# Performance work log

Hardware: AMD Instinct MI355X
Metric: run time of the kernel (lower is better)

## Reference

```python
import jax, jax.numpy as jnp
import numpy as np

B, C, HEADS, D, DKQ = 1024, 512, 8, 64, 8
DV = C // HEADS                 # 64, dim_head_v
QKVC = DV + 2 * DKQ             # 80, qkv channels per head
EPS = 1e-5


def _bn(x, g, b, m, v):
    # eval-mode batchnorm, channel axis = 1
    shp = (1, -1) + (1,) * (x.ndim - 2)
    scale = g.reshape(shp) / jnp.sqrt(v.reshape(shp) + EPS)
    return (x - m.reshape(shp)) * scale + b.reshape(shp)


def _rel_index():
    i = np.arange(D)
    # key_index - query_index + D - 1, row-major flatten -> (D*D,)
    return jnp.asarray((i[:, None] - i[None, :] + D - 1).reshape(-1))


def setup_inputs() -> dict:
    key = jax.random.key(0)
    ks = jax.random.split(key, 16)
    O = HEADS * QKVC
    d = {
        "x": jax.random.normal(ks[0], (B, C, D), jnp.float32),
        "conv_w": jax.random.normal(ks[1], (O, C), jnp.float32) * 0.02,
        "bn1_g": jax.random.normal(ks[2], (O,), jnp.float32) * 0.1 + 1.0,
        "bn1_b": jax.random.normal(ks[3], (O,), jnp.float32) * 0.1,
        "bn1_m": jax.random.normal(ks[4], (O,), jnp.float32) * 0.1,
        "bn1_v": jax.random.uniform(ks[5], (O,), jnp.float32) * 0.5 + 0.5,
        "rel": jax.random.normal(ks[6], (QKVC, 2 * D - 1), jnp.float32),
        "bn2_g": jax.random.normal(ks[7], (3 * HEADS,), jnp.float32) * 0.1 + 1.0,
        "bn2_b": jax.random.normal(ks[8], (3 * HEADS,), jnp.float32) * 0.1,
        "bn2_m": jax.random.normal(ks[9], (3 * HEADS,), jnp.float32) * 0.1,
        "bn2_v": jax.random.uniform(ks[10], (3 * HEADS,), jnp.float32) * 0.5 + 0.5,
        "bn3_g": jax.random.normal(ks[11], (2 * C,), jnp.float32) * 0.1 + 1.0,
        "bn3_b": jax.random.normal(ks[12], (2 * C,), jnp.float32) * 0.1,
        "bn3_m": jax.random.normal(ks[13], (2 * C,), jnp.float32) * 0.1,
        "bn3_v": jax.random.uniform(ks[14], (2 * C,), jnp.float32) * 0.5 + 0.5,
    }
    return d


def reference(x, conv_w, bn1_g, bn1_b, bn1_m, bn1_v, rel,
              bn2_g, bn2_b, bn2_m, bn2_v, bn3_g, bn3_b, bn3_m, bn3_v):
    # 1x1 conv1d + BN1d: [B, O, D]
    qkv = jnp.einsum('oc,bcd->bod', conv_w, x)
    qkv = _bn(qkv, bn1_g, bn1_b, bn1_m, bn1_v)
    # rearrange 'b (q h) d -> b h q d' with q=QKVC, h=HEADS (channel = q*H + h)
    qkv = qkv.reshape(B, QKVC, HEADS, D).transpose(0, 2, 1, 3)  # [B,H,QKVC,D]
    q = qkv[:, :, :DKQ]                # [B,H,DKQ,D]
    k = qkv[:, :, DKQ:2 * DKQ]         # [B,H,DKQ,D]
    v = qkv[:, :, 2 * DKQ:]            # [B,H,DV,D]

    # relative positional embeddings gathered from table
    emb = rel[:, _rel_index()].reshape(QKVC, D, D)
    r_q, r_k, r_v = emb[:DKQ], emb[DKQ:2 * DKQ], emb[2 * DKQ:]

    qr = jnp.einsum('bhid,idj->bhdj', q, r_q)
    kr = jnp.einsum('bhid,idj->bhdj', k, r_k)
    dots = jnp.einsum('bhid,bhij->bhdj', q, k)

    # rearrange 'n b h d j -> b (h n) d j'  (channel = h*3 + n)
    stacked = jnp.stack([qr, kr, dots], axis=2).reshape(B, 3 * HEADS, D, D)
    stacked = _bn(stacked, bn2_g, bn2_b, bn2_m, bn2_v)
    norm_dots = stacked.reshape(B, HEADS, 3, D, D).sum(axis=2)  # [B,H,D,D]

    attn = jax.nn.softmax(norm_dots, axis=-1)
    out = jnp.einsum('bhdj,bhij->bhid', attn, v)      # [B,H,DV,D]
    kv = jnp.einsum('bhdj,idj->bhid', attn, r_v)      # [B,H,DV,D]

    # rearrange 'n b h i d -> b (n h i) d'  (channel = n*H*DV + h*DV + i)
    st = jnp.stack([kv, out], axis=1).reshape(B, 2 * HEADS * DV, D)
    st = _bn(st, bn3_g, bn3_b, bn3_m, bn3_v)
    return st.reshape(B, 2, HEADS * DV, D).sum(axis=1)  # [B,C,D]
```

## Files before the change

kernel.cpp:

```cpp
#include <hip/hip_runtime.h>
#include <hip/hip_bf16.h>

#define B_    1024
#define C_    512
#define H_    8
#define D_    64
#define EPS_  1e-5f

typedef __attribute__((ext_vector_type(4))) float f32x4;
typedef __attribute__((ext_vector_type(8))) short bf16x8;
typedef __attribute__((ext_vector_type(8))) unsigned short u16x8;

__device__ __forceinline__ float bf2f(unsigned short h) {
    union { unsigned int u; float f; } c;
    c.u = ((unsigned int)h) << 16;
    return c.f;
}
__device__ __forceinline__ unsigned short f2bf(float f) {
    __hip_bfloat16 h = __float2bfloat16(f);
    return *reinterpret_cast<unsigned short*>(&h);
}

__global__ __launch_bounds__(256) void k0_wconv(
    const float* __restrict__ w, unsigned short* __restrict__ wf)
{
    int t = blockIdx.x * 256 + threadIdx.x;
    int o  = t >> 6;
    int c0 = (t & 63) * 8;
    const float* src = w + (size_t)o * C_ + c0;
    u16x8 p;
#pragma unroll
    for (int e = 0; e < 8; ++e) p[e] = f2bf(src[e]);
    int f = (o >> 4) * 16 + (c0 >> 5);
    int l = (o & 15) | (((c0 >> 3) & 3) << 4);
    *reinterpret_cast<u16x8*>(&wf[(size_t)f * 512 + l * 8]) = p;
}

__global__ __launch_bounds__(256) void k0_tables(
    const float* __restrict__ rel,
    const float* __restrict__ g2, const float* __restrict__ v2,
    const float* __restrict__ g3, const float* __restrict__ v3,
    unsigned short* __restrict__ relB, unsigned short* __restrict__ relvA)
{
    int tid = blockIdx.x * 256 + threadIdx.x;
    if (tid < 4096) {
        int h = tid >> 9, uf = (tid >> 6) & 7, l = tid & 63;
        int u = uf * 16 + (l & 15);
        int g = l >> 4;
        float sq = g2[3*h]     * rsqrtf(v2[3*h]     + EPS_);
        float sk = g2[3*h + 1] * rsqrtf(v2[3*h + 1] + EPS_);
        u16x8 p;
#pragma unroll
        for (int e = 0; e < 8; ++e) {
            int s = g * 8 + e;
            float val = 0.f;
            if (u < 127 && s < 16)
                val = (s < 8 ? sq : sk) * rel[s * 127 + u];
            p[e] = f2bf(val);
        }
        *reinterpret_cast<u16x8*>(&relB[(size_t)tid * 8]) = p;
    } else if (tid < 4096 + 8192) {
        int t2 = tid - 4096;
        int h = t2 >> 10, iF = (t2 >> 8) & 3, tt = (t2 >> 6) & 3, l = t2 & 63;
        int i = iF * 16 + (l & 15);
        int c3 = h * 64 + i;
        float scl = g3[c3] * rsqrtf(v3[c3] + EPS_);
        const float* rrow = rel + (size_t)(16 + i) * 127;
        u16x8 p;
#pragma unroll
        for (int e = 0; e < 8; ++e) {
            int u = (l >> 4) * 8 + e + 32 * tt;
            p[e] = f2bf((u < 127) ? scl * rrow[u] : 0.f);
        }
        *reinterpret_cast<u16x8*>(&relvA[(size_t)t2 * 8]) = p;
    }
}

#define LDW1 40

__global__ __launch_bounds__(512) void k1_gemm(
    const float* __restrict__ x, const unsigned short* __restrict__ wf,
    const float* __restrict__ g1, const float* __restrict__ b1,
    const float* __restrict__ m1, const float* __restrict__ v1,
    const float* __restrict__ g3, const float* __restrict__ v3,
    unsigned short* __restrict__ qkA, unsigned short* __restrict__ vB)
{
    __shared__ unsigned short xt[32 * LDW1];
    __shared__ float ssc[640], ssh[640];

    const int tid = threadIdx.x;
    const int b   = blockIdx.x >> 1;
    const int dh  = blockIdx.x & 1;
    const int d0  = dh * 32;

    for (int t = tid; t < 640; t += 512) {
        float sc = g1[t] * rsqrtf(v1[t] + EPS_);
        float sh = b1[t] - m1[t] * sc;
        int cc = t >> 3, hh = t & 7;
        if (cc >= 16) {
            int c3 = 512 + hh * 64 + (cc - 16);
            float f = g3[c3] * rsqrtf(v3[c3] + EPS_);
            sc *= f; sh *= f;
        }
        ssc[t] = sc;
        ssh[t] = sh;
    }

    const int lane = tid & 63;
    const int wv   = tid >> 6;
    const int wrow = wv * 80;
    const int lm   = lane & 15;
    const int lk   = (lane >> 4) * 8;

    f32x4 acc[5][2];
#pragma unroll
    for (int i = 0; i < 5; ++i)
#pragma unroll
        for (int j = 0; j < 2; ++j) acc[i][j] = (f32x4){0.f, 0.f, 0.f, 0.f};

    const float* xb = x + (size_t)b * C_ * D_;
    const int skp = tid >> 5;
    const int sdd = tid & 31;

    for (int kk = 0; kk < C_; kk += 32) {
        __syncthreads();
        bf16x8 af[5];
#pragma unroll
        for (int fm = 0; fm < 5; ++fm) {
            size_t f = (size_t)((wv * 5 + fm) * 16 + (kk >> 5)) * 512;
            af[fm] = *reinterpret_cast<const bf16x8*>(&wf[f + lane * 8]);
        }
        {
            float a0 = xb[(kk + 2 * skp) * 64 + d0 + sdd];
            float a1 = xb[(kk + 2 * skp + 1) * 64 + d0 + sdd];
            unsigned int pk = (unsigned int)f2bf(a0) | ((unsigned int)f2bf(a1) << 16);
            *reinterpret_cast<unsigned int*>(&xt[sdd * LDW1 + 2 * skp]) = pk;
        }
        __syncthreads();

        bf16x8 bfr[2];
#pragma unroll
        for (int fn = 0; fn < 2; ++fn)
            bfr[fn] = *reinterpret_cast<const bf16x8*>(&xt[(fn * 16 + lm) * LDW1 + lk]);
#pragma unroll
        for (int fm = 0; fm < 5; ++fm)
#pragma unroll
            for (int fn = 0; fn < 2; ++fn)
                acc[fm][fn] = __builtin_amdgcn_mfma_f32_16x16x32_bf16(
                    af[fm], bfr[fn], acc[fm][fn], 0, 0, 0);
    }

    const int r0 = (lane >> 4) * 4;
#pragma unroll
    for (int fm = 0; fm < 5; ++fm) {
#pragma unroll
        for (int fn = 0; fn < 2; ++fn) {
            int d = d0 + fn * 16 + lm;
#pragma unroll
            for (int r = 0; r < 4; ++r) {
                int o = wrow + fm * 16 + r0 + r;
                int cc = o >> 3, hh = o & 7;
                float val = acc[fm][fn][r] * ssc[o] + ssh[o];
                unsigned short bv = f2bf(val);
                if (cc < 8)
                    qkA[(((size_t)b * 8 + hh) * 4 + (d >> 4)) * 512 + (d & 15) * 8 + cc] = bv;
                else if (cc < 16)
                    qkA[(((size_t)b * 8 + hh) * 4 + (d >> 4)) * 512 + ((d & 15) + 16) * 8 + (cc - 8)] = bv;
                else
                    vB[((size_t)(b * 8 + hh) * 64 + (cc - 16)) * 64 + d] = bv;
            }
        }
    }
    for (int z = tid; z < 2048; z += 512) {
        int hm  = z >> 7;
        int off = z & 127;
        int hh  = hm >> 1;
        int mf  = dh * 2 + (hm & 1);
        unsigned int* p = reinterpret_cast<unsigned int*>(
            qkA + (((size_t)b * 8 + hh) * 4 + mf) * 512 + 256);
        p[off] = 0u;
    }
}

#define SGP 84
#define SA  72
#define RLD 136

__global__ __launch_bounds__(256) void k2_attn(
    const unsigned short* __restrict__ qkA, const unsigned short* __restrict__ vB,
    const unsigned short* __restrict__ relB, const unsigned short* __restrict__ relvA,
    const float* __restrict__ g2, const float* __restrict__ v2,
    const float* __restrict__ g3, const float* __restrict__ b3,
    const float* __restrict__ m3, const float* __restrict__ v3,
    float* __restrict__ outp)
{
    __shared__ float          SGb[64 * SGP];
    __shared__ unsigned short attn[64 * SA];
    __shared__ unsigned short A2[64 * RLD];
    __shared__ float sh3[64];

    const int tid  = threadIdx.x;
    const int b    = blockIdx.x >> 3;
    const int h    = blockIdx.x & 7;
    const int lane = tid & 63;
    const int w    = tid >> 6;
    const int lmm  = lane & 15;
    const int lg   = lane >> 4;

    const unsigned short* qbase = qkA + ((size_t)(b * 8 + h) * 4) * 512;

    for (int i = tid; i < 64 * RLD / 2; i += 256)
        reinterpret_cast<unsigned int*>(A2)[i] = 0u;
    if (tid < 64) {
        int c = h * 64 + tid;
        float sa = g3[c] * rsqrtf(v3[c] + EPS_);
        float sb = g3[512 + c] * rsqrtf(v3[512 + c] + EPS_);
        sh3[tid] = (b3[c] - m3[c] * sa) + (b3[512 + c] - m3[512 + c] * sb);
    }
    const float s_dt = g2[3 * h + 2] * rsqrtf(v2[3 * h + 2] + EPS_);

    bf16x8 aA = *reinterpret_cast<const bf16x8*>(&qbase[w * 512 + lane * 8]);
    bf16x8 zv = {0, 0, 0, 0, 0, 0, 0, 0};
    bf16x8 kBf[4];
#pragma unroll
    for (int jf = 0; jf < 4; ++jf) {
        kBf[jf] = zv;
        if (lane < 16)
            kBf[jf] = *reinterpret_cast<const bf16x8*>(&qbase[jf * 512 + (lane + 16) * 8]);
    }
    bf16x8 rBf[8];
#pragma unroll
    for (int uf = 0; uf < 8; ++uf)
        rBf[uf] = *reinterpret_cast<const bf16x8*>(&relB[(size_t)(h * 8 + uf) * 512 + lane * 8]);

    f32x4 dotsAcc[4];
#pragma unroll
    for (int jf = 0; jf < 4; ++jf)
        dotsAcc[jf] = __builtin_amdgcn_mfma_f32_16x16x32_bf16(
            aA, kBf[jf], (f32x4){0.f, 0.f, 0.f, 0.f}, 0, 0, 0);
    f32x4 sgAcc[8];
#pragma unroll
    for (int uf = 0; uf < 8; ++uf)
        sgAcc[uf] = __builtin_amdgcn_mfma_f32_16x16x32_bf16(
            aA, rBf[uf], (f32x4){0.f, 0.f, 0.f, 0.f}, 0, 0, 0);

#pragma unroll
    for (int uf = 0; uf < 8; ++uf) {
#pragma unroll
        for (int r = 0; r < 4; ++r) {
            int d = (w << 4) + (lg << 2) + r;
            int t = uf * 16 + lmm - d + 15;
            if (t >= 0 && t < 79)
                SGb[d * SGP + t] = sgAcc[uf][r];
        }
    }
    __syncthreads();

#pragma unroll
    for (int r = 0; r < 4; ++r) {
        int d = (w << 4) + (lg << 2) + r;
        const float* sgr = &SGb[d * SGP];
        float sc0 = s_dt * dotsAcc[0][r] + sgr[78 - lmm];
        float sc1 = s_dt * dotsAcc[1][r] + sgr[62 - lmm];
        float sc2 = s_dt * dotsAcc[2][r] + sgr[46 - lmm];
        float sc3 = s_dt * dotsAcc[3][r] + sgr[30 - lmm];
        float mx = fmaxf(fmaxf(sc0, sc1), fmaxf(sc2, sc3));
        mx = fmaxf(mx, __shfl_xor(mx, 1));
        mx = fmaxf(mx, __shfl_xor(mx, 2));
        mx = fmaxf(mx, __shfl_xor(mx, 4));
        mx = fmaxf(mx, __shfl_xor(mx, 8));
        float e0 = __expf(sc0 - mx), e1 = __expf(sc1 - mx);
        float e2 = __expf(sc2 - mx), e3 = __expf(sc3 - mx);
        float sum = (e0 + e1) + (e2 + e3);
        sum += __shfl_xor(sum, 1);
        sum += __shfl_xor(sum, 2);
        sum += __shfl_xor(sum, 4);
        sum += __shfl_xor(sum, 8);
        float inv = 1.f / sum;
        unsigned short p0 = f2bf(e0 * inv), p1 = f2bf(e1 * inv);
        unsigned short p2 = f2bf(e2 * inv), p3 = f2bf(e3 * inv);
        attn[d * SA + lmm]      = p0;
        attn[d * SA + 16 + lmm] = p1;
        attn[d * SA + 32 + lmm] = p2;
        attn[d * SA + 48 + lmm] = p3;
        A2[d * RLD + 63 + d - lmm] = p0;
        A2[d * RLD + 47 + d - lmm] = p1;
        A2[d * RLD + 31 + d - lmm] = p2;
        A2[d * RLD + 15 + d - lmm] = p3;
    }

    const int lk8  = lg * 8;
    const int irow = (w << 4) + lmm;
    const unsigned short* vbase = vB + (size_t)(b * 8 + h) * 4096;
    bf16x8 av0 = *reinterpret_cast<const bf16x8*>(&vbase[irow * 64 + lk8]);
    bf16x8 av1 = *reinterpret_cast<const bf16x8*>(&vbase[irow * 64 + 32 + lk8]);
    bf16x8 rvA[4];
#pragma unroll
    for (int t = 0; t < 4; ++t)
        rvA[t] = *reinterpret_cast<const bf16x8*>(
            &relvA[(size_t)(((h * 4 + w) * 4 + t)) * 512 + lane * 8]);

    __syncthreads();

    f32x4 acc[4];
#pragma unroll
    for (int nf = 0; nf < 4; ++nf) acc[nf] = (f32x4){0.f, 0.f, 0.f, 0.f};

#pragma unroll
    for (int nf = 0; nf < 4; ++nf) {
        const unsigned short* arow = &attn[(nf * 16 + lmm) * SA + lk8];
        acc[nf] = __builtin_amdgcn_mfma_f32_16x16x32_bf16(
            av0, *reinterpret_cast<const bf16x8*>(&arow[0]), acc[nf], 0, 0, 0);
        acc[nf] = __builtin_amdgcn_mfma_f32_16x16x32_bf16(
            av1, *reinterpret_cast<const bf16x8*>(&arow[32]), acc[nf], 0, 0, 0);
        const unsigned short* a2row = &A2[(nf * 16 + lmm) * RLD + lk8];
        acc[nf] = __builtin_amdgcn_mfma_f32_16x16x32_bf16(
            rvA[0], *reinterpret_cast<const bf16x8*>(&a2row[0]), acc[nf], 0, 0, 0);
        acc[nf] = __builtin_amdgcn_mfma_f32_16x16x32_bf16(
            rvA[1], *reinterpret_cast<const bf16x8*>(&a2row[32]), acc[nf], 0, 0, 0);
        acc[nf] = __builtin_amdgcn_mfma_f32_16x16x32_bf16(
            rvA[2], *reinterpret_cast<const bf16x8*>(&a2row[64]), acc[nf], 0, 0, 0);
        acc[nf] = __builtin_amdgcn_mfma_f32_16x16x32_bf16(
            rvA[3], *reinterpret_cast<const bf16x8*>(&a2row[96]), acc[nf], 0, 0, 0);
    }

    float* op = outp + ((size_t)b * 512 + h * 64) * 64;
    const int r0 = lg * 4;
#pragma unroll
    for (int r = 0; r < 4; ++r) {
        int i = (w << 4) + r0 + r;
        float sh = sh3[i];
#pragma unroll
        for (int nf = 0; nf < 4; ++nf)
            op[(size_t)i * 64 + nf * 16 + lmm] = acc[nf][r] + sh;
    }
}

extern "C" void kernel_launch(void* const* d_in, const int* in_sizes, int n_in,
                              void* d_out, int out_size, void* d_ws, size_t ws_size,
                              hipStream_t stream) {
    (void)in_sizes; (void)n_in; (void)out_size; (void)ws_size;
    const float* x   = (const float*)d_in[0];
    const float* w   = (const float*)d_in[1];
    const float* g1  = (const float*)d_in[2];
    const float* b1  = (const float*)d_in[3];
    const float* m1  = (const float*)d_in[4];
    const float* v1  = (const float*)d_in[5];
    const float* rel = (const float*)d_in[6];
    const float* g2  = (const float*)d_in[7];
    const float* b2  = (const float*)d_in[8];  (void)b2;
    const float* m2  = (const float*)d_in[9];  (void)m2;
    const float* v2  = (const float*)d_in[10];
    const float* g3  = (const float*)d_in[11];
    const float* b3  = (const float*)d_in[12];
    const float* m3  = (const float*)d_in[13];
    const float* v3  = (const float*)d_in[14];
    float* out = (float*)d_out;

    unsigned short* wfrag = (unsigned short*)d_ws;
    unsigned short* relB  = (unsigned short*)((char*)d_ws + 655360);
    unsigned short* relvA = (unsigned short*)((char*)d_ws + 720896);
    unsigned short* qkA   = (unsigned short*)((char*)d_ws + 1048576);
    unsigned short* vB    = (unsigned short*)((char*)d_ws + 1048576 + (size_t)33554432);

    hipLaunchKernelGGL(k0_wconv, dim3(160), dim3(256), 0, stream, w, wfrag);
    hipLaunchKernelGGL(k0_tables, dim3(48), dim3(256), 0, stream,
                       rel, g2, v2, g3, v3, relB, relvA);
    hipLaunchKernelGGL(k1_gemm, dim3(2048), dim3(512), 0, stream,
                       x, wfrag, g1, b1, m1, v1, g3, v3, qkA, vB);
    hipLaunchKernelGGL(k2_attn, dim3(8192), dim3(256), 0, stream,
                       qkA, vB, relB, relvA, g2, v2, g3, b3, m3, v3, out);
}
```

Measured before the change: 203.4 us.

## Widen k1 GEMM tile to full D per block with double-buffered LDS prefetch

The projection GEMM now has each block cover all 64 positions of a batch instead of half. The weight fragments loaded per k-step are therefore reused across twice as many MFMAs, and the grid is halved. The K loop moves to 64-wide steps with a double-buffered LDS tile. The next x tile is prefetched into registers with vectorized float4 loads while the current one is computed, which cuts barriers per K. In exchange, accumulator registers double, which may lower occupancy, and there are fewer blocks to spread across the CUs.

```diff
diff --git a/kernel.cpp b/kernel.cpp
--- a/kernel.cpp
+++ b/kernel.cpp
@@ -76,7 +76,7 @@
     }
 }
 
-#define LDW1 40
+#define LDW1 72
 
 __global__ __launch_bounds__(512) void k1_gemm(
     const float* __restrict__ x, const unsigned short* __restrict__ wf,
@@ -85,13 +85,11 @@
     const float* __restrict__ g3, const float* __restrict__ v3,
     unsigned short* __restrict__ qkA, unsigned short* __restrict__ vB)
 {
-    __shared__ unsigned short xt[32 * LDW1];
+    __shared__ unsigned short xt[2][64 * LDW1];
     __shared__ float ssc[640], ssh[640];
 
     const int tid = threadIdx.x;
-    const int b   = blockIdx.x >> 1;
-    const int dh  = blockIdx.x & 1;
-    const int d0  = dh * 32;
+    const int b   = blockIdx.x;
 
     for (int t = tid; t < 640; t += 512) {
         float sc = g1[t] * rsqrtf(v1[t] + EPS_);
@@ -108,57 +106,76 @@
 
     const int lane = tid & 63;
     const int wv   = tid >> 6;
-    const int wrow = wv * 80;
     const int lm   = lane & 15;
-    const int lk   = (lane >> 4) * 8;
-
-    f32x4 acc[5][2];
+    const int lg   = lane >> 4;
+
+    const float* xb = x + (size_t)b * C_ * D_;
+    const int cp = tid >> 4;
+    const int c4 = (tid & 15) * 4;
+
+    f32x4 acc[5][4];
 #pragma unroll
     for (int i = 0; i < 5; ++i)
 #pragma unroll
-        for (int j = 0; j < 2; ++j) acc[i][j] = (f32x4){0.f, 0.f, 0.f, 0.f};
-
-    const float* xb = x + (size_t)b * C_ * D_;
-    const int skp = tid >> 5;
-    const int sdd = tid & 31;
-
-    for (int kk = 0; kk < C_; kk += 32) {
+        for (int j = 0; j < 4; ++j) acc[i][j] = (f32x4){0.f, 0.f, 0.f, 0.f};
+
+    {
+        f32x4 a = *reinterpret_cast<const f32x4*>(&xb[(2 * cp) * 64 + c4]);
+        f32x4 c = *reinterpret_cast<const f32x4*>(&xb[(2 * cp + 1) * 64 + c4]);
+#pragma unroll
+        for (int j = 0; j < 4; ++j) {
+            unsigned int pk = (unsigned int)f2bf(a[j]) | ((unsigned int)f2bf(c[j]) << 16);
+            *reinterpret_cast<unsigned int*>(&xt[0][(c4 + j) * LDW1 + 2 * cp]) = pk;
+        }
+    }
+    __syncthreads();
+
+    int cur = 0;
+    for (int kt = 0; kt < 8; ++kt) {
+        f32x4 pa, pc;
+        if (kt < 7) {
+            pa = *reinterpret_cast<const f32x4*>(&xb[((kt + 1) * 64 + 2 * cp) * 64 + c4]);
+            pc = *reinterpret_cast<const f32x4*>(&xb[((kt + 1) * 64 + 2 * cp + 1) * 64 + c4]);
+        }
+#pragma unroll
+        for (int ks = 0; ks < 2; ++ks) {
+            bf16x8 af[5];
+#pragma unroll
+            for (int fm = 0; fm < 5; ++fm) {
+                size_t f = (size_t)((wv * 5 + fm) * 16 + kt * 2 + ks) * 512;
+                af[fm] = *reinterpret_cast<const bf16x8*>(&wf[f + lane * 8]);
+            }
+            bf16x8 bfr[4];
+#pragma unroll
+            for (int fn = 0; fn < 4; ++fn)
+                bfr[fn] = *reinterpret_cast<const bf16x8*>(
+                    &xt[cur][(fn * 16 + lm) * LDW1 + ks * 32 + lg * 8]);
+#pragma unroll
+            for (int fm = 0; fm < 5; ++fm)
+#pragma unroll
+                for (int fn = 0; fn < 4; ++fn)
+                    acc[fm][fn] = __builtin_amdgcn_mfma_f32_16x16x32_bf16(
+                        af[fm], bfr[fn], acc[fm][fn], 0, 0, 0);
+        }
+        if (kt < 7) {
+#pragma unroll
+            for (int j = 0; j < 4; ++j) {
+                unsigned int pk = (unsigned int)f2bf(pa[j]) | ((unsigned int)f2bf(pc[j]) << 16);
+                *reinterpret_cast<unsigned int*>(&xt[cur ^ 1][(c4 + j) * LDW1 + 2 * cp]) = pk;
+            }
+        }
         __syncthreads();
-        bf16x8 af[5];
-#pragma unroll
-        for (int fm = 0; fm < 5; ++fm) {
-            size_t f = (size_t)((wv * 5 + fm) * 16 + (kk >> 5)) * 512;
-            af[fm] = *reinterpret_cast<const bf16x8*>(&wf[f + lane * 8]);
-        }
-        {
-            float a0 = xb[(kk + 2 * skp) * 64 + d0 + sdd];
-            float a1 = xb[(kk + 2 * skp + 1) * 64 + d0 + sdd];
-            unsigned int pk = (unsigned int)f2bf(a0) | ((unsigned int)f2bf(a1) << 16);
-            *reinterpret_cast<unsigned int*>(&xt[sdd * LDW1 + 2 * skp]) = pk;
-        }
-        __syncthreads();
-
-        bf16x8 bfr[2];
-#pragma unroll
-        for (int fn = 0; fn < 2; ++fn)
-            bfr[fn] = *reinterpret_cast<const bf16x8*>(&xt[(fn * 16 + lm) * LDW1 + lk]);
-#pragma unroll
-        for (int fm = 0; fm < 5; ++fm)
-#pragma unroll
-            for (int fn = 0; fn < 2; ++fn)
-                acc[fm][fn] = __builtin_amdgcn_mfma_f32_16x16x32_bf16(
-                    af[fm], bfr[fn], acc[fm][fn], 0, 0, 0);
-    }
-
-    const int r0 = (lane >> 4) * 4;
+        cur ^= 1;
+    }
+
 #pragma unroll
     for (int fm = 0; fm < 5; ++fm) {
 #pragma unroll
-        for (int fn = 0; fn < 2; ++fn) {
-            int d = d0 + fn * 16 + lm;
+        for (int fn = 0; fn < 4; ++fn) {
+            int d = fn * 16 + lm;
 #pragma unroll
             for (int r = 0; r < 4; ++r) {
-                int o = wrow + fm * 16 + r0 + r;
+                int o = wv * 80 + fm * 16 + lg * 4 + r;
                 int cc = o >> 3, hh = o & 7;
                 float val = acc[fm][fn][r] * ssc[o] + ssh[o];
                 unsigned short bv = f2bf(val);
@@ -171,11 +188,10 @@
             }
         }
     }
-    for (int z = tid; z < 2048; z += 512) {
-        int hm  = z >> 7;
+    for (int z = tid; z < 4096; z += 512) {
+        int hh  = z >> 9;
+        int mf  = (z >> 7) & 3;
         int off = z & 127;
-        int hh  = hm >> 1;
-        int mf  = dh * 2 + (hm & 1);
         unsigned int* p = reinterpret_cast<unsigned int*>(
             qkA + (((size_t)b * 8 + hh) * 4 + mf) * 512 + 256);
         p[off] = 0u;
@@ -366,7 +382,7 @@
     hipLaunchKernelGGL(k0_wconv, dim3(160), dim3(256), 0, stream, w, wfrag);
     hipLaunchKernelGGL(k0_tables, dim3(48), dim3(256), 0, stream,
                        rel, g2, v2, g3, v3, relB, relvA);
-    hipLaunchKernelGGL(k1_gemm, dim3(2048), dim3(512), 0, stream,
+    hipLaunchKernelGGL(k1_gemm, dim3(1024), dim3(512), 0, stream,
                        x, wfrag, g1, b1, m1, v1, g3, v3, qkA, vB);
     hipLaunchKernelGGL(k2_attn, dim3(8192), dim3(256), 0, stream,
                        qkA, vB, relB, relvA, g2, v2, g3, b3, m3, v3, out);
```

New measurement: 192.1 us. 5.5% less time.

## Double-buffer k1 GEMM tiles, split rows across blocks, compact qkA layout

Applied to the files above, without the earlier changes.

The conv GEMM kernel now uses 256-thread blocks that each cover half of the 640 output rows, so twice as many blocks are launched. The K loop is fully unrolled with register double-buffering of weight fragments and an LDS double buffer for x, prefetching the next tile while MFMAs run. It also uses a single barrier per step with an explicit lgkmcnt wait. The qkA layout drops the zero-padded upper half of each fragment, halving that buffer and removing the zero-fill pass; the attention kernel instead zero-fills the missing lanes in registers. In exchange, the x tile is read from global twice as often, and the hand-written barrier must keep LDS ordering correct.

```diff
diff --git a/kernel.cpp b/kernel.cpp
--- a/kernel.cpp
+++ b/kernel.cpp
@@ -7,6 +7,7 @@
 #define D_    64
 #define EPS_  1e-5f
 
+typedef __attribute__((ext_vector_type(2))) float f32x2;
 typedef __attribute__((ext_vector_type(4))) float f32x4;
 typedef __attribute__((ext_vector_type(8))) short bf16x8;
 typedef __attribute__((ext_vector_type(8))) unsigned short u16x8;
@@ -20,6 +21,11 @@
     __hip_bfloat16 h = __float2bfloat16(f);
     return *reinterpret_cast<unsigned short*>(&h);
 }
+
+#define KBAR() do { \
+    asm volatile("s_waitcnt lgkmcnt(0)" ::: "memory"); \
+    __builtin_amdgcn_s_barrier(); \
+} while (0)
 
 __global__ __launch_bounds__(256) void k0_wconv(
     const float* __restrict__ w, unsigned short* __restrict__ wf)
@@ -78,25 +84,73 @@
 
 #define LDW1 40
 
-__global__ __launch_bounds__(512) void k1_gemm(
+struct K1Ctx {
+    const float* xb;
+    const unsigned short* wfw;
+    unsigned short (*xt)[32 * LDW1];
+    int lm, lg, cp, d2l, dcol0;
+};
+
+template<int KT>
+__device__ __forceinline__ void k1_step(const K1Ctx& c, f32x4 (&acc)[5][2],
+                                        bf16x8 (&afu)[5], bf16x8 (&afp)[5])
+{
+    if (KT < 15) {
+#pragma unroll
+        for (int fm = 0; fm < 5; ++fm)
+            afp[fm] = *reinterpret_cast<const bf16x8*>(
+                &c.wfw[(size_t)(fm * 16 + KT + 1) * 512]);
+    }
+    f32x2 pa, pb;
+    if (KT < 15) {
+        pa = *reinterpret_cast<const f32x2*>(
+            &c.xb[((KT + 1) * 32 + 2 * c.cp) * 64 + c.dcol0 + c.d2l]);
+        pb = *reinterpret_cast<const f32x2*>(
+            &c.xb[((KT + 1) * 32 + 2 * c.cp + 1) * 64 + c.dcol0 + c.d2l]);
+    }
+    bf16x8 bfr[2];
+#pragma unroll
+    for (int fn = 0; fn < 2; ++fn)
+        bfr[fn] = *reinterpret_cast<const bf16x8*>(
+            &c.xt[KT & 1][(fn * 16 + c.lm) * LDW1 + c.lg * 8]);
+#pragma unroll
+    for (int fm = 0; fm < 5; ++fm)
+#pragma unroll
+        for (int fn = 0; fn < 2; ++fn)
+            acc[fm][fn] = __builtin_amdgcn_mfma_f32_16x16x32_bf16(
+                afu[fm], bfr[fn], acc[fm][fn], 0, 0, 0);
+    if (KT < 15) {
+        unsigned int p0 = (unsigned int)f2bf(pa[0]) | ((unsigned int)f2bf(pb[0]) << 16);
+        unsigned int p1 = (unsigned int)f2bf(pa[1]) | ((unsigned int)f2bf(pb[1]) << 16);
+        *reinterpret_cast<unsigned int*>(
+            &c.xt[(KT & 1) ^ 1][c.d2l * LDW1 + 2 * c.cp]) = p0;
+        *reinterpret_cast<unsigned int*>(
+            &c.xt[(KT & 1) ^ 1][(c.d2l + 1) * LDW1 + 2 * c.cp]) = p1;
+    }
+    KBAR();
+}
+
+__global__ __launch_bounds__(256, 4) void k1_gemm(
     const float* __restrict__ x, const unsigned short* __restrict__ wf,
     const float* __restrict__ g1, const float* __restrict__ b1,
     const float* __restrict__ m1, const float* __restrict__ v1,
     const float* __restrict__ g3, const float* __restrict__ v3,
     unsigned short* __restrict__ qkA, unsigned short* __restrict__ vB)
 {
-    __shared__ unsigned short xt[32 * LDW1];
-    __shared__ float ssc[640], ssh[640];
-
-    const int tid = threadIdx.x;
-    const int b   = blockIdx.x >> 1;
-    const int dh  = blockIdx.x & 1;
-    const int d0  = dh * 32;
-
-    for (int t = tid; t < 640; t += 512) {
-        float sc = g1[t] * rsqrtf(v1[t] + EPS_);
-        float sh = b1[t] - m1[t] * sc;
-        int cc = t >> 3, hh = t & 7;
+    __shared__ unsigned short xt[2][32 * LDW1];
+    __shared__ float ssc[320], ssh[320];
+
+    const int tid  = threadIdx.x;
+    const int b    = blockIdx.x >> 2;
+    const int mh   = (blockIdx.x >> 1) & 1;
+    const int dh   = blockIdx.x & 1;
+    const int row0 = mh * 320;
+
+    for (int t = tid; t < 320; t += 256) {
+        int o = row0 + t;
+        float sc = g1[o] * rsqrtf(v1[o] + EPS_);
+        float sh = b1[o] - m1[o] * sc;
+        int cc = o >> 3, hh = o & 7;
         if (cc >= 16) {
             int c3 = 512 + hh * 64 + (cc - 16);
             float f = g3[c3] * rsqrtf(v3[c3] + EPS_);
@@ -108,9 +162,16 @@
 
     const int lane = tid & 63;
     const int wv   = tid >> 6;
-    const int wrow = wv * 80;
-    const int lm   = lane & 15;
-    const int lk   = (lane >> 4) * 8;
+
+    K1Ctx c;
+    c.xb    = x + (size_t)b * C_ * D_;
+    c.wfw   = wf + (size_t)(mh * 20 + wv * 5) * 16 * 512 + lane * 8;
+    c.xt    = xt;
+    c.lm    = lane & 15;
+    c.lg    = lane >> 4;
+    c.cp    = tid >> 4;
+    c.d2l   = (tid & 15) * 2;
+    c.dcol0 = dh * 32;
 
     f32x4 acc[5][2];
 #pragma unroll
@@ -118,67 +179,60 @@
 #pragma unroll
         for (int j = 0; j < 2; ++j) acc[i][j] = (f32x4){0.f, 0.f, 0.f, 0.f};
 
-    const float* xb = x + (size_t)b * C_ * D_;
-    const int skp = tid >> 5;
-    const int sdd = tid & 31;
-
-    for (int kk = 0; kk < C_; kk += 32) {
-        __syncthreads();
-        bf16x8 af[5];
-#pragma unroll
-        for (int fm = 0; fm < 5; ++fm) {
-            size_t f = (size_t)((wv * 5 + fm) * 16 + (kk >> 5)) * 512;
-            af[fm] = *reinterpret_cast<const bf16x8*>(&wf[f + lane * 8]);
-        }
-        {
-            float a0 = xb[(kk + 2 * skp) * 64 + d0 + sdd];
-            float a1 = xb[(kk + 2 * skp + 1) * 64 + d0 + sdd];
-            unsigned int pk = (unsigned int)f2bf(a0) | ((unsigned int)f2bf(a1) << 16);
-            *reinterpret_cast<unsigned int*>(&xt[sdd * LDW1 + 2 * skp]) = pk;
-        }
-        __syncthreads();
-
-        bf16x8 bfr[2];
-#pragma unroll
-        for (int fn = 0; fn < 2; ++fn)
-            bfr[fn] = *reinterpret_cast<const bf16x8*>(&xt[(fn * 16 + lm) * LDW1 + lk]);
-#pragma unroll
-        for (int fm = 0; fm < 5; ++fm)
-#pragma unroll
-            for (int fn = 0; fn < 2; ++fn)
-                acc[fm][fn] = __builtin_amdgcn_mfma_f32_16x16x32_bf16(
-                    af[fm], bfr[fn], acc[fm][fn], 0, 0, 0);
-    }
-
-    const int r0 = (lane >> 4) * 4;
+    bf16x8 afA[5], afB[5];
+#pragma unroll
+    for (int fm = 0; fm < 5; ++fm)
+        afA[fm] = *reinterpret_cast<const bf16x8*>(&c.wfw[(size_t)(fm * 16) * 512]);
+    {
+        f32x2 a = *reinterpret_cast<const f32x2*>(
+            &c.xb[(2 * c.cp) * 64 + c.dcol0 + c.d2l]);
+        f32x2 d = *reinterpret_cast<const f32x2*>(
+            &c.xb[(2 * c.cp + 1) * 64 + c.dcol0 + c.d2l]);
+        unsigned int p0 = (unsigned int)f2bf(a[0]) | ((unsigned int)f2bf(d[0]) << 16);
+        unsigned int p1 = (unsigned int)f2bf(a[1]) | ((unsigned int)f2bf(d[1]) << 16);
+        *reinterpret_cast<unsigned int*>(&xt[0][c.d2l * LDW1 + 2 * c.cp]) = p0;
+        *reinterpret_cast<unsigned int*>(&xt[0][(c.d2l + 1) * LDW1 + 2 * c.cp]) = p1;
+    }
+    KBAR();
+
+    k1_step< 0>(c, acc, afA, afB);
+    k1_step< 1>(c, acc, afB, afA);
+    k1_step< 2>(c, acc, afA, afB);
+    k1_step< 3>(c, acc, afB, afA);
+    k1_step< 4>(c, acc, afA, afB);
+    k1_step< 5>(c, acc, afB, afA);
+    k1_step< 6>(c, acc, afA, afB);
+    k1_step< 7>(c, acc, afB, afA);
+    k1_step< 8>(c, acc, afA, afB);
+    k1_step< 9>(c, acc, afB, afA);
+    k1_step<10>(c, acc, afA, afB);
+    k1_step<11>(c, acc, afB, afA);
+    k1_step<12>(c, acc, afA, afB);
+    k1_step<13>(c, acc, afB, afA);
+    k1_step<14>(c, acc, afA, afB);
+    k1_step<15>(c, acc, afB, afA);
+
+    const int lm = c.lm, lg = c.lg;
 #pragma unroll
     for (int fm = 0; fm < 5; ++fm) {
 #pragma unroll
         for (int fn = 0; fn < 2; ++fn) {
-            int d = d0 + fn * 16 + lm;
+            int d = dh * 32 + fn * 16 + lm;
 #pragma unroll
             for (int r = 0; r < 4; ++r) {
-                int o = wrow + fm * 16 + r0 + r;
+                int rl = wv * 80 + fm * 16 + lg * 4 + r;
+                int o  = row0 + rl;
                 int cc = o >> 3, hh = o & 7;
-                float val = acc[fm][fn][r] * ssc[o] + ssh[o];
+                float val = acc[fm][fn][r] * ssc[rl] + ssh[rl];
                 unsigned short bv = f2bf(val);
                 if (cc < 8)
-                    qkA[(((size_t)b * 8 + hh) * 4 + (d >> 4)) * 512 + (d & 15) * 8 + cc] = bv;
+                    qkA[(((size_t)b * 8 + hh) * 4 + (d >> 4)) * 256 + (d & 15) * 8 + cc] = bv;
                 else if (cc < 16)
-                    qkA[(((size_t)b * 8 + hh) * 4 + (d >> 4)) * 512 + ((d & 15) + 16) * 8 + (cc - 8)] = bv;
+                    qkA[(((size_t)b * 8 + hh) * 4 + (d >> 4)) * 256 + ((d & 15) + 16) * 8 + (cc - 8)] = bv;
                 else
                     vB[((size_t)(b * 8 + hh) * 64 + (cc - 16)) * 64 + d] = bv;
             }
         }
-    }
-    for (int z = tid; z < 2048; z += 512) {
-        int hm  = z >> 7;
-        int off = z & 127;
-        int hh  = hm >> 1;
-        int mf  = dh * 2 + (hm & 1);
-        unsigned int* p = reinterpret_cast<unsigned int*>(
-            qkA + (((size_t)b * 8 + hh) * 4 + mf) * 512 + 256);
-        p[off] = 0u;
     }
 }
 
@@ -207,7 +261,7 @@
     const int lmm  = lane & 15;
     const int lg   = lane >> 4;
 
-    const unsigned short* qbase = qkA + ((size_t)(b * 8 + h) * 4) * 512;
+    const unsigned short* qbase = qkA + ((size_t)(b * 8 + h) * 4) * 256;
 
     for (int i = tid; i < 64 * RLD / 2; i += 256)
         reinterpret_cast<unsigned int*>(A2)[i] = 0u;
@@ -219,14 +273,16 @@
     }
     const float s_dt = g2[3 * h + 2] * rsqrtf(v2[3 * h + 2] + EPS_);
 
-    bf16x8 aA = *reinterpret_cast<const bf16x8*>(&qbase[w * 512 + lane * 8]);
     bf16x8 zv = {0, 0, 0, 0, 0, 0, 0, 0};
+    bf16x8 aA = zv;
+    if (lane < 32)
+        aA = *reinterpret_cast<const bf16x8*>(&qbase[w * 256 + lane * 8]);
     bf16x8 kBf[4];
 #pragma unroll
     for (int jf = 0; jf < 4; ++jf) {
         kBf[jf] = zv;
         if (lane < 16)
-            kBf[jf] = *reinterpret_cast<const bf16x8*>(&qbase[jf * 512 + (lane + 16) * 8]);
+            kBf[jf] = *reinterpret_cast<const bf16x8*>(&qbase[jf * 256 + (lane + 16) * 8]);
     }
     bf16x8 rBf[8];
 #pragma unroll
@@ -361,12 +417,12 @@
     unsigned short* relB  = (unsigned short*)((char*)d_ws + 655360);
     unsigned short* relvA = (unsigned short*)((char*)d_ws + 720896);
     unsigned short* qkA   = (unsigned short*)((char*)d_ws + 1048576);
-    unsigned short* vB    = (unsigned short*)((char*)d_ws + 1048576 + (size_t)33554432);
+    unsigned short* vB    = (unsigned short*)((char*)d_ws + 1048576 + (size_t)16777216);
 
     hipLaunchKernelGGL(k0_wconv, dim3(160), dim3(256), 0, stream, w, wfrag);
     hipLaunchKernelGGL(k0_tables, dim3(48), dim3(256), 0, stream,
                        rel, g2, v2, g3, v3, relB, relvA);
-    hipLaunchKernelGGL(k1_gemm, dim3(2048), dim3(512), 0, stream,
+    hipLaunchKernelGGL(k1_gemm, dim3(4096), dim3(256), 0, stream,
                        x, wfrag, g1, b1, m1, v1, g3, v3, qkA, vB);
     hipLaunchKernelGGL(k2_attn, dim3(8192), dim3(256), 0, stream,
                        qkA, vB, relB, relvA, g2, v2, g3, b3, m3, v3, out);
```

After: 214.0 us. 5.2% more time.
